# Performance work log

Hardware: AMD Instinct MI355X
Metric: run time of the kernel (lower is better)

The kernel has to match this reference:

```python
import jax, jax.numpy as jnp
import numpy as np

B, S, IN, E, H, NL = 64, 512, 1024, 128, 8, 4
D = E // H  # head dim = 16


def setup_inputs() -> dict:
    key = jax.random.key(0)
    ks = jax.random.split(key, 12)
    rn = lambda k, shape: jax.random.normal(k, shape, jnp.float32) * 0.02
    x = jax.random.normal(ks[0], (B, S, IN), jnp.float32)
    # per-recording valid lengths; recording 0 full-length so no attention key row is all-masked
    lengths = jax.random.randint(ks[1], (B,), 1, S + 1).at[0].set(S)
    key_padding_mask = jnp.arange(S)[None, :] >= lengths[:, None]  # (B,S) True = pad
    return {
        'x': x,
        'key_padding_mask': key_padding_mask,
        'embed_w': rn(ks[2], (IN, E)), 'embed_b': jnp.zeros((E,), jnp.float32),
        'qkv_w': rn(ks[3], (NL, 3, E, E)), 'qkv_b': jnp.zeros((NL, 3, E), jnp.float32),
        'out_w': rn(ks[4], (NL, E, E)), 'out_b': jnp.zeros((NL, E), jnp.float32),
        'ln_g': jnp.ones((NL, E), jnp.float32), 'ln_b': jnp.zeros((NL, E), jnp.float32),
        'ff1_w': rn(ks[5], (NL, E, 4 * E)), 'ff1_b': jnp.zeros((NL, 4 * E), jnp.float32),
        'ff2_w': rn(ks[6], (NL, 4 * E, E)), 'ff2_b': jnp.zeros((NL, E), jnp.float32),
        'fc1_w': rn(ks[7], (E, 32)), 'fc1_b': jnp.zeros((32,), jnp.float32),
        'fc2_w': rn(ks[8], (32, 1)), 'fc2_b': jnp.zeros((1,), jnp.float32),
    }


def _ln(x, g, b):
    m = x.mean(-1, keepdims=True)
    v = x.var(-1, keepdims=True)
    return (x - m) / jnp.sqrt(v + 1e-5) * g + b


def _pos_enc(s, e):
    pos = jnp.arange(s, dtype=jnp.float32)[:, None]
    i = jnp.arange(e)[None, :]
    angle = pos / jnp.power(jnp.float32(10000.0), (2 * (i // 2)).astype(jnp.float32) / e)
    return jnp.where(i % 2 == 0, jnp.sin(angle), jnp.cos(angle))  # (S,E)


def reference(x, key_padding_mask, embed_w, embed_b, qkv_w, qkv_b, out_w, out_b,
              ln_g, ln_b, ff1_w, ff1_b, ff2_w, ff2_b, fc1_w, fc1_b, fc2_w, fc2_b):
    h = x @ embed_w + embed_b  # (B,S,E)
    pe = _pos_enc(S, E)
    scale = 1.0 / jnp.sqrt(jnp.float32(D))
    # module uses batch_first=False MHA on (B,S,E): attention runs across recordings.
    # key_padding_mask.T -> (S,B): masked keys are recordings, per epoch position.
    keymask = key_padding_mask.T[:, None, None, :]  # (S,1,1,B)
    for l in range(NL):
        h = h + pe[None]  # pos enc re-added every block (as in source)
        res = h
        q = (h @ qkv_w[l, 0] + qkv_b[l, 0]).reshape(B, S, H, D)
        k = (h @ qkv_w[l, 1] + qkv_b[l, 1]).reshape(B, S, H, D)
        v = (h @ qkv_w[l, 2] + qkv_b[l, 2]).reshape(B, S, H, D)
        scores = jnp.einsum('ishd,jshd->shij', q, k) * scale  # (S,H,B,B)
        scores = jnp.where(keymask, -jnp.inf, scores)
        attn = jax.nn.softmax(scores, axis=-1)
        o = jnp.einsum('shij,jshd->ishd', attn, v).reshape(B, S, E)
        o = o @ out_w[l] + out_b[l]
        h = _ln(o + res, ln_g[l], ln_b[l])
        res = h
        ffo = jax.nn.relu(h @ ff1_w[l] + ff1_b[l]) @ ff2_w[l] + ff2_b[l]
        h = _ln(ffo + res, ln_g[l], ln_b[l])  # same LN params reused, as in source
    # masked mean pool over epochs (vectorized replacement of the python loop)
    valid = (~key_padding_mask).astype(h.dtype)  # (B,S)
    mean = jnp.einsum('bse,bs->be', h, valid) / valid.sum(axis=1)[:, None]
    out = jax.nn.relu(mean @ fc1_w + fc1_b) @ fc2_w + fc2_b  # (B,1)
    return jax.nn.sigmoid(out)
```

## Files before the change

### kernel.cpp

```cpp
#include <hip/hip_runtime.h>

#define Bb 64
#define Ss 512
#define INn 1024
#define Ee 128
#define Hh 8
#define Dd 16
#define NLl 4

typedef unsigned short u16;
typedef __attribute__((ext_vector_type(8))) short short8;
typedef __attribute__((ext_vector_type(4))) float f32x4;

__device__ __forceinline__ float b2f(unsigned u) { return __uint_as_float(u << 16); }
__device__ __forceinline__ u16 f2b(float f) {
    unsigned u = __float_as_uint(f);
    unsigned r = u + 0x7FFFu + ((u >> 16) & 1u);
    return (u16)(r >> 16);
}
__device__ __forceinline__ uint2 pk4(float4 f) {
    uint2 r;
    r.x = (unsigned)f2b(f.x) | ((unsigned)f2b(f.y) << 16);
    r.y = (unsigned)f2b(f.z) | ((unsigned)f2b(f.w) << 16);
    return r;
}

#define GLOAD_LDS16(g, l) __builtin_amdgcn_global_load_lds( \
    (const __attribute__((address_space(1))) void*)(g),     \
    (__attribute__((address_space(3))) void*)(l), 16, 0, 0)

#define MFMA16(a, b, c) __builtin_amdgcn_mfma_f32_16x16x32_bf16((a), (b), (c), 0, 0, 0)

__global__ __launch_bounds__(256) void prep_kernel(const unsigned char* __restrict__ m,
                                                   int* __restrict__ lengths,
                                                   float* __restrict__ pe,
                                                   const float* __restrict__ ew,
                                                   const float* __restrict__ qw,
                                                   const float* __restrict__ ow,
                                                   const float* __restrict__ f1w,
                                                   const float* __restrict__ f2w,
                                                   u16* __restrict__ we, u16* __restrict__ wq,
                                                   u16* __restrict__ wo, u16* __restrict__ wf1,
                                                   u16* __restrict__ wf2) {
    const int bid = blockIdx.x, tid = threadIdx.x;
    if (bid == 0) {
        __shared__ int lf[3];
        __shared__ int part[256];
        if (tid < 3) lf[tid] = 0;
        __syncthreads();
        int l0 = 0, l1 = 0, l23 = 0;
        for (int i = tid * 128; i < tid * 128 + 128; ++i) {
            if (m[i]) { int md = i & 3; if (md == 0) l0 = 1; else if (md == 1) l1 = 1; else l23 = 1; }
        }
        if (l0) atomicOr(&lf[0], 1);
        if (l1) atomicOr(&lf[1], 1);
        if (l23) atomicOr(&lf[2], 1);
        __syncthreads();
        int enc = lf[1] ? 1 : (lf[2] ? 2 : 0);
        int b = tid >> 2, q = tid & 3, cnt = 0;
        for (int s = q * 128; s < q * 128 + 128; ++s) {
            int idx = b * Ss + s;
            int mm;
            if (enc == 1)      mm = (m[idx] != 0);
            else if (enc == 2) mm = (((const float*)(const void*)m)[idx] != 0.0f);
            else               mm = (((const int*)(const void*)m)[idx] != 0);
            cnt += (mm == 0);
        }
        part[tid] = cnt;
        __syncthreads();
        if (tid < 64)
            lengths[tid] = part[tid * 4] + part[tid * 4 + 1] + part[tid * 4 + 2] + part[tid * 4 + 3];
        return;
    }
    if (bid <= 32) {
        for (int i = tid; i < 2048; i += 256) {
            int idx = (bid - 1) * 2048 + i;
            int s = idx >> 7, e = idx & 127;
            float expo = (float)(2 * (e >> 1)) * (1.0f / 128.0f);
            float freq = powf(10000.0f, -expo);
            float angle = (float)s * freq;
            pe[idx] = (e & 1) ? cosf(angle) : sinf(angle);
        }
        return;
    }
    int tb = bid - 33;
    const float* src; u16* dst; int K, N, tile;
    if (tb < 32)       { src = ew;  dst = we;  K = 1024; N = 128; tile = tb; }
    else if (tb < 80)  { int b = tb - 32;  int mat = b >> 2; src = qw  + (size_t)mat * 16384; dst = wq  + (size_t)mat * 16384; K = 128; N = 128; tile = b & 3; }
    else if (tb < 96)  { int b = tb - 80;  int mat = b >> 2; src = ow  + (size_t)mat * 16384; dst = wo  + (size_t)mat * 16384; K = 128; N = 128; tile = b & 3; }
    else if (tb < 160) { int b = tb - 96;  int mat = b >> 4; src = f1w + (size_t)mat * 65536; dst = wf1 + (size_t)mat * 65536; K = 128; N = 512; tile = b & 15; }
    else               { int b = tb - 160; int mat = b >> 4; src = f2w + (size_t)mat * 65536; dst = wf2 + (size_t)mat * 65536; K = 512; N = 128; tile = b & 15; }
    int ktiles = K >> 6;
    int k0 = (tile % ktiles) * 64, n0 = (tile / ktiles) * 64;
    __shared__ __align__(16) u16 t_s[64 * 68];
    int r = tid >> 2, cq = (tid & 3) * 16;
    const float* sp = src + (size_t)(k0 + r) * N + n0 + cq;
#pragma unroll
    for (int i = 0; i < 4; ++i) {
        float4 f = *(const float4*)(sp + 4 * i);
        *(uint2*)&t_s[r * 68 + cq + 4 * i] = pk4(f);
    }
    __syncthreads();
    u16 tmp[16];
#pragma unroll
    for (int kk = 0; kk < 16; ++kk) tmp[kk] = t_s[(cq + kk) * 68 + r];
    int rowg = n0 + r;
    int x = (rowg & 7) << 3;
    u16* base = dst + (size_t)rowg * K;
    *(uint4*)(base + ((k0 + cq) ^ x))     = ((uint4*)tmp)[0];
    *(uint4*)(base + ((k0 + cq + 8) ^ x)) = ((uint4*)tmp)[1];
}

__global__ __launch_bounds__(256) void embed_gemm(const float* __restrict__ X,
                                                  const u16* __restrict__ Wt,
                                                  const float* __restrict__ bias,
                                                  const float* __restrict__ pe,
                                                  u16* __restrict__ C) {
    __shared__ __align__(16) u16 Af[64 * 68];
    __shared__ __align__(16) u16 Bs[2][128 * 64];
    const int tid = threadIdx.x;
    const int w = tid >> 6, lane = tid & 63, l16 = lane & 15, lhi = lane >> 4;
    const int row0 = blockIdx.x * 64;
    const int xr = (l16 & 7) << 3;
    f32x4 acc[8];
#pragma unroll
    for (int ni = 0; ni < 8; ++ni) acc[ni] = (f32x4){0.f, 0.f, 0.f, 0.f};

    const int ar = tid >> 2, ak = (tid & 3) * 16;
    const int crow = tid >> 3, cc8 = (tid & 7) * 8;
    const int wave_lds = w * 512;
    const u16* Bbase = Wt + cc8;
    const float* Arow = X + (size_t)(row0 + ar) * 1024 + ak;

#pragma unroll
    for (int i = 0; i < 4; ++i)
        GLOAD_LDS16(Bbase + (size_t)(i * 32 + crow) * 1024, &Bs[0][i * 2048 + wave_lds]);

    for (int it = 0; it < 16; ++it) {
        const int k0 = it * 64;
        __syncthreads();
#pragma unroll
        for (int i = 0; i < 4; ++i) {
            float4 f = *(const float4*)(Arow + k0 + 4 * i);
            *(uint2*)&Af[ar * 68 + ak + 4 * i] = pk4(f);
        }
        __syncthreads();
        if (it < 15) {
#pragma unroll
            for (int i = 0; i < 4; ++i)
                GLOAD_LDS16(Bbase + (size_t)(i * 32 + crow) * 1024 + k0 + 64,
                            &Bs[(it + 1) & 1][i * 2048 + wave_lds]);
        }
#pragma unroll
        for (int ks = 0; ks < 2; ++ks) {
            short8 af;
            ((uint2*)&af)[0] = *(const uint2*)&Af[(w * 16 + l16) * 68 + ks * 32 + lhi * 8];
            ((uint2*)&af)[1] = *(const uint2*)&Af[(w * 16 + l16) * 68 + ks * 32 + lhi * 8 + 4];
#pragma unroll
            for (int ni = 0; ni < 8; ++ni) {
                short8 bfr = *(const short8*)&Bs[it & 1][(ni * 16 + l16) * 64 + ((ks * 32 + lhi * 8) ^ xr)];
                acc[ni] = MFMA16(af, bfr, acc[ni]);
            }
        }
    }
    float biasr[8];
#pragma unroll
    for (int ni = 0; ni < 8; ++ni) biasr[ni] = bias[ni * 16 + l16];
#pragma unroll
    for (int reg = 0; reg < 4; ++reg) {
        int r = row0 + w * 16 + lhi * 4 + reg;
        int s = r & 511;
        int bidx = r >> 9;
        int orow = s * 64 + bidx;
        int xo = (bidx & 7) << 3;
        const float* per = pe + (size_t)s * 128;
        u16* crw = C + (size_t)orow * 128;
#pragma unroll
        for (int ni = 0; ni < 8; ++ni) {
            int c = ni * 16 + l16;
            crw[c ^ xo] = f2b(acc[ni][reg] + biasr[ni] + per[c]);
        }
    }
}

__global__ __launch_bounds__(256) void qkv_gemm(const u16* __restrict__ A,
                                                const u16* __restrict__ Wt,
                                                const float* __restrict__ bias,
                                                u16* __restrict__ Cq,
                                                u16* __restrict__ Ckv) {
    __shared__ __align__(16) u16 As[128 * 128];
    __shared__ __align__(16) u16 Bs[128 * 128];
    const int tid = threadIdx.x, w = tid >> 6, lane = tid & 63;
    const int l16 = lane & 15, lhi = lane >> 4;
    const int row0 = blockIdx.x * 128, col0 = blockIdx.y * 128;
    const int so = w * 512 + lane * 8;
    const int xr = (l16 & 7) << 3;
#pragma unroll
    for (int i = 0; i < 8; ++i) {
        GLOAD_LDS16(A + (size_t)row0 * 128 + i * 2048 + so, &As[i * 2048 + w * 512]);
        GLOAD_LDS16(Wt + (size_t)col0 * 128 + i * 2048 + so, &Bs[i * 2048 + w * 512]);
    }
    __syncthreads();
    f32x4 acc[2][8];
#pragma unroll
    for (int mi = 0; mi < 2; ++mi)
#pragma unroll
        for (int ni = 0; ni < 8; ++ni) acc[mi][ni] = (f32x4){0.f, 0.f, 0.f, 0.f};
#pragma unroll
    for (int ks = 0; ks < 4; ++ks) {
        const int ko = (ks * 32 + lhi * 8) ^ xr;
        short8 af[2], bfr[8];
#pragma unroll
        for (int mi = 0; mi < 2; ++mi)
            af[mi] = *(const short8*)&As[(w * 32 + mi * 16 + l16) * 128 + ko];
#pragma unroll
        for (int ni = 0; ni < 8; ++ni)
            bfr[ni] = *(const short8*)&Bs[(ni * 16 + l16) * 128 + ko];
#pragma unroll
        for (int mi = 0; mi < 2; ++mi)
#pragma unroll
            for (int ni = 0; ni < 8; ++ni)
                acc[mi][ni] = MFMA16(af[mi], bfr[ni], acc[mi][ni]);
    }
    float biasr[8];
#pragma unroll
    for (int ni = 0; ni < 8; ++ni) biasr[ni] = bias[col0 + ni * 16 + l16];
#pragma unroll
    for (int mi = 0; mi < 2; ++mi)
#pragma unroll
        for (int reg = 0; reg < 4; ++reg) {
            int r = row0 + w * 32 + mi * 16 + lhi * 4 + reg;
            u16* crw; int cbase;
            if (col0 == 0) { crw = Cq + (size_t)r * 128; cbase = 0; }
            else           { crw = Ckv + (size_t)r * 256; cbase = col0 - 128; }
#pragma unroll
            for (int ni = 0; ni < 8; ++ni)
                crw[cbase + ni * 16 + l16] = f2b(acc[mi][ni][reg] + biasr[ni]);
        }
}

__global__ __launch_bounds__(256) void attnout_kernel(const u16* __restrict__ qb,
                                                      const u16* __restrict__ kvb,
                                                      const u16* __restrict__ wo,
                                                      const float* __restrict__ outb,
                                                      const int* __restrict__ lengths,
                                                      const float* __restrict__ gamma,
                                                      const float* __restrict__ beta,
                                                      u16* __restrict__ h) {
    const int s = blockIdx.x;
    const int tid = threadIdx.x, w = tid >> 6, lane = tid & 63;
    const int l16 = lane & 15, lhi = lane >> 4;
    __shared__ __align__(16) u16 Ps[4 * 64 * 72];
    __shared__ __align__(16) u16 o_s[64 * 136];
    __shared__ int len_s[64];

    if (tid < 64) len_s[tid] = lengths[tid];
    __syncthreads();

    bool mk[4];
#pragma unroll
    for (int jt = 0; jt < 4; ++jt) mk[jt] = (s >= len_s[jt * 16 + l16]);

    u16* pw = Ps + w * 4608;
#pragma unroll
    for (int hp = 0; hp < 2; ++hp) {
        const int hh = w * 2 + hp;
        short8 af[4];
#pragma unroll
        for (int it = 0; it < 4; ++it) {
            af[it] = (short8){0, 0, 0, 0, 0, 0, 0, 0};
            if (lhi < 2)
                af[it] = *(const short8*)(qb + ((size_t)(s * 64 + it * 16 + l16)) * 128 + hh * 16 + lhi * 8);
        }
        f32x4 sf[4][4];
#pragma unroll
        for (int jt = 0; jt < 4; ++jt) {
            short8 bf = (short8){0, 0, 0, 0, 0, 0, 0, 0};
            if (lhi < 2)
                bf = *(const short8*)(kvb + ((size_t)(s * 64 + jt * 16 + l16)) * 256 + hh * 16 + lhi * 8);
#pragma unroll
            for (int it = 0; it < 4; ++it) {
                f32x4 z = {0.f, 0.f, 0.f, 0.f};
                sf[it][jt] = MFMA16(af[it], bf, z);
            }
        }
        float inv[4][4];
#pragma unroll
        for (int it = 0; it < 4; ++it) {
#pragma unroll
            for (int reg = 0; reg < 4; ++reg) {
                float vv[4], mx = -1e30f;
#pragma unroll
                for (int jt = 0; jt < 4; ++jt) {
                    float xv = mk[jt] ? -1e30f : sf[it][jt][reg] * 0.25f;
                    vv[jt] = xv; mx = fmaxf(mx, xv);
                }
                mx = fmaxf(mx, __shfl_xor(mx, 1)); mx = fmaxf(mx, __shfl_xor(mx, 2));
                mx = fmaxf(mx, __shfl_xor(mx, 4)); mx = fmaxf(mx, __shfl_xor(mx, 8));
                float e4[4], sum = 0.f;
#pragma unroll
                for (int jt = 0; jt < 4; ++jt) {
                    float e = mk[jt] ? 0.f : __expf(vv[jt] - mx);
                    e4[jt] = e; sum += e;
                }
                sum += __shfl_xor(sum, 1); sum += __shfl_xor(sum, 2);
                sum += __shfl_xor(sum, 4); sum += __shfl_xor(sum, 8);
                inv[it][reg] = 1.0f / sum;
                int prow = it * 16 + lhi * 4 + reg;
#pragma unroll
                for (int jt = 0; jt < 4; ++jt)
                    pw[prow * 72 + jt * 16 + l16] = f2b(e4[jt]);
            }
        }
        f32x4 ao[4];
#pragma unroll
        for (int it = 0; it < 4; ++it) ao[it] = (f32x4){0.f, 0.f, 0.f, 0.f};
        short8 vb[2];
#pragma unroll
        for (int ksv = 0; ksv < 2; ++ksv)
#pragma unroll
            for (int e = 0; e < 8; ++e)
                vb[ksv][e] = (short)kvb[((size_t)(s * 64 + ksv * 32 + lhi * 8 + e)) * 256
                                        + 128 + hh * 16 + l16];
#pragma unroll
        for (int it = 0; it < 4; ++it)
#pragma unroll
            for (int ksv = 0; ksv < 2; ++ksv) {
                short8 pa = *(const short8*)&pw[(it * 16 + l16) * 72 + ksv * 32 + lhi * 8];
                ao[it] = MFMA16(pa, vb[ksv], ao[it]);
            }
#pragma unroll
        for (int it = 0; it < 4; ++it)
#pragma unroll
            for (int reg = 0; reg < 4; ++reg)
                o_s[(it * 16 + lhi * 4 + reg) * 136 + hh * 16 + l16] = f2b(ao[it][reg] * inv[it][reg]);
    }
    __syncthreads();

    const int xr = (l16 & 7) << 3;
    f32x4 acc[8];
#pragma unroll
    for (int ni = 0; ni < 8; ++ni) acc[ni] = (f32x4){0.f, 0.f, 0.f, 0.f};
#pragma unroll
    for (int ks = 0; ks < 4; ++ks) {
        short8 af = *(const short8*)&o_s[(w * 16 + l16) * 136 + ks * 32 + lhi * 8];
#pragma unroll
        for (int ni = 0; ni < 8; ++ni) {
            short8 bf = *(const short8*)(wo + (size_t)(ni * 16 + l16) * 128 + ((ks * 32 + lhi * 8) ^ xr));
            acc[ni] = MFMA16(af, bf, acc[ni]);
        }
    }
    float biasr[8], gr[8], br[8];
#pragma unroll
    for (int ni = 0; ni < 8; ++ni) {
        int c = ni * 16 + l16;
        biasr[ni] = outb[c]; gr[ni] = gamma[c]; br[ni] = beta[c];
    }
#pragma unroll
    for (int reg = 0; reg < 4; ++reg) {
        int row = w * 16 + lhi * 4 + reg;
        int xo = (row & 7) << 3;
        size_t rbase = ((size_t)(s * 64 + row)) * 128;
        float v[8], sm = 0.f, s2 = 0.f;
#pragma unroll
        for (int ni = 0; ni < 8; ++ni) {
            float x = acc[ni][reg] + biasr[ni] + b2f(h[rbase + ((ni * 16 + l16) ^ xo)]);
            v[ni] = x; sm += x; s2 += x * x;
        }
        sm += __shfl_xor(sm, 1); sm += __shfl_xor(sm, 2);
        sm += __shfl_xor(sm, 4); sm += __shfl_xor(sm, 8);
        s2 += __shfl_xor(s2, 1); s2 += __shfl_xor(s2, 2);
        s2 += __shfl_xor(s2, 4); s2 += __shfl_xor(s2, 8);
        float mean = sm * (1.0f / 128.0f);
        float var = s2 * (1.0f / 128.0f) - mean * mean;
        float rstd = rsqrtf(fmaxf(var, 0.0f) + 1e-5f);
#pragma unroll
        for (int ni = 0; ni < 8; ++ni)
            h[rbase + ((ni * 16 + l16) ^ xo)] = f2b((v[ni] - mean) * rstd * gr[ni] + br[ni]);
    }
}

__global__ __launch_bounds__(256) void ff_fused(const u16* __restrict__ hbuf,
                                                const u16* __restrict__ w1t,
                                                const u16* __restrict__ w2t,
                                                const float* __restrict__ b1,
                                                const float* __restrict__ b2,
                                                const float* __restrict__ gamma,
                                                const float* __restrict__ beta,
                                                const float* __restrict__ pe,
                                                u16* __restrict__ hout) {
    __shared__ __align__(16) u16 A_s[8192];
    __shared__ __align__(16) u16 W1_s[8192];
    __shared__ __align__(16) u16 W2_s[8192];
    __shared__ __align__(16) u16 T_s[4096];
    const int tid = threadIdx.x, w = tid >> 6, lane = tid & 63;
    const int l16 = lane & 15, lhi = lane >> 4;
    const int row0 = blockIdx.x * 64;
    const int so = w * 512 + lane * 8;
    const int xr = (l16 & 7) << 3;

#pragma unroll
    for (int i = 0; i < 4; ++i)
        GLOAD_LDS16(hbuf + (size_t)row0 * 128 + i * 2048 + so, &A_s[i * 2048 + w * 512]);
#pragma unroll
    for (int i = 0; i < 4; ++i) {
        int slot = i * 2048 + so;
        GLOAD_LDS16(w1t + (size_t)(slot >> 7) * 128 + ((slot & 127) ^ (((slot >> 7) & 7) << 3)),
                    &W1_s[slot]);
        GLOAD_LDS16(w2t + (size_t)(slot >> 6) * 512 + ((slot & 63) ^ (((slot >> 6) & 7) << 3)),
                    &W2_s[slot]);
    }
    __syncthreads();

    f32x4 acc2[8];
#pragma unroll
    for (int ni = 0; ni < 8; ++ni) acc2[ni] = (f32x4){0.f, 0.f, 0.f, 0.f};

    for (int nc = 0; nc < 8; ++nc) {
        f32x4 acc1[4];
#pragma unroll
        for (int ni = 0; ni < 4; ++ni) acc1[ni] = (f32x4){0.f, 0.f, 0.f, 0.f};
#pragma unroll
        for (int ks = 0; ks < 4; ++ks) {
            const int ko = (ks * 32 + lhi * 8) ^ xr;
            short8 af = *(const short8*)&A_s[(w * 16 + l16) * 128 + ko];
#pragma unroll
            for (int ni = 0; ni < 4; ++ni) {
                short8 bf = *(const short8*)&W1_s[(ni * 16 + l16) * 128 + ko];
                acc1[ni] = MFMA16(af, bf, acc1[ni]);
            }
        }
        float bb[4];
#pragma unroll
        for (int ni = 0; ni < 4; ++ni) bb[ni] = b1[nc * 64 + ni * 16 + l16];
#pragma unroll
        for (int reg = 0; reg < 4; ++reg) {
            int xt = ((lhi * 4 + reg) & 7) << 3;
#pragma unroll
            for (int ni = 0; ni < 4; ++ni)
                T_s[(w * 16 + lhi * 4 + reg) * 64 + ((ni * 16 + l16) ^ xt)] =
                    f2b(fmaxf(acc1[ni][reg] + bb[ni], 0.0f));
        }
        __syncthreads();
        if (nc < 7) {
#pragma unroll
            for (int i = 0; i < 4; ++i) {
                int slot = i * 2048 + so;
                GLOAD_LDS16(w1t + (size_t)((nc + 1) * 64 + (slot >> 7)) * 128
                                + ((slot & 127) ^ (((slot >> 7) & 7) << 3)),
                            &W1_s[slot]);
            }
        }
#pragma unroll
        for (int ks = 0; ks < 2; ++ks) {
            const int ko = (ks * 32 + lhi * 8) ^ xr;
            short8 pa = *(const short8*)&T_s[(w * 16 + l16) * 64 + ko];
#pragma unroll
            for (int ni = 0; ni < 8; ++ni) {
                short8 bf = *(const short8*)&W2_s[(ni * 16 + l16) * 64 + ko];
                acc2[ni] = MFMA16(pa, bf, acc2[ni]);
            }
        }
        __syncthreads();
        if (nc < 7) {
#pragma unroll
            for (int i = 0; i < 4; ++i) {
                int slot = i * 2048 + so;
                GLOAD_LDS16(w2t + (size_t)(slot >> 6) * 512 + (nc + 1) * 64
                                + ((slot & 63) ^ (((slot >> 6) & 7) << 3)),
                            &W2_s[slot]);
            }
        }
    }
    float b2r[8], gr[8], br[8];
#pragma unroll
    for (int ni = 0; ni < 8; ++ni) {
        int c = ni * 16 + l16;
        b2r[ni] = b2[c]; gr[ni] = gamma[c]; br[ni] = beta[c];
    }
#pragma unroll
    for (int reg = 0; reg < 4; ++reg) {
        int lrow = w * 16 + lhi * 4 + reg;
        int r = row0 + lrow;
        int xo = (lrow & 7) << 3;
        float v[8], sm = 0.f, s2 = 0.f;
#pragma unroll
        for (int ni = 0; ni < 8; ++ni) {
            float x = acc2[ni][reg] + b2r[ni] + b2f(A_s[lrow * 128 + ((ni * 16 + l16) ^ xo)]);
            v[ni] = x; sm += x; s2 += x * x;
        }
        sm += __shfl_xor(sm, 1); sm += __shfl_xor(sm, 2);
        sm += __shfl_xor(sm, 4); sm += __shfl_xor(sm, 8);
        s2 += __shfl_xor(s2, 1); s2 += __shfl_xor(s2, 2);
        s2 += __shfl_xor(s2, 4); s2 += __shfl_xor(s2, 8);
        float mean = sm * (1.0f / 128.0f);
        float var = s2 * (1.0f / 128.0f) - mean * mean;
        float rstd = rsqrtf(fmaxf(var, 0.0f) + 1e-5f);
        u16* crw = hout + (size_t)r * 128;
#pragma unroll
        for (int ni = 0; ni < 8; ++ni) {
            int c = ni * 16 + l16;
            float val = (v[ni] - mean) * rstd * gr[ni] + br[ni];
            if (pe) val += pe[(size_t)(r >> 6) * 128 + c];
            crw[c ^ xo] = f2b(val);
        }
    }
}

__global__ __launch_bounds__(256) void poolhead_kernel(const u16* __restrict__ h,
                                                       const int* __restrict__ lengths,
                                                       const float* __restrict__ fc1w,
                                                       const float* __restrict__ fc1b,
                                                       const float* __restrict__ fc2w,
                                                       const float* __restrict__ fc2b,
                                                       float* __restrict__ out) {
    int b = blockIdx.x, tid = threadIdx.x;
    int e = tid & 127, half = tid >> 7;
    int len = lengths[b];
    int ep = e ^ ((b & 7) << 3);
    float s = 0.0f;
    for (int t = half; t < len; t += 2) s += b2f(h[((size_t)(t * 64 + b)) * 128 + ep]);
    __shared__ float red[256];
    __shared__ float mp[128];
    __shared__ float z[32];
    red[tid] = s;
    __syncthreads();
    if (tid < 128) mp[tid] = (red[tid] + red[tid + 128]) / (float)len;
    __syncthreads();
    if (tid < 32) {
        float a = fc1b[tid];
        for (int k = 0; k < 128; ++k) a = fmaf(mp[k], fc1w[k * 32 + tid], a);
        z[tid] = fmaxf(a, 0.0f);
    }
    __syncthreads();
    if (tid == 0) {
        float a = fc2b[0];
#pragma unroll
        for (int t = 0; t < 32; ++t) a = fmaf(z[t], fc2w[t], a);
        out[b] = 1.0f / (1.0f + expf(-a));
    }
}

extern "C" void kernel_launch(void* const* d_in, const int* in_sizes, int n_in,
                              void* d_out, int out_size, void* d_ws, size_t ws_size,
                              hipStream_t stream) {
    (void)in_sizes; (void)n_in; (void)out_size; (void)ws_size;
    const float* x        = (const float*)d_in[0];
    const unsigned char* mask = (const unsigned char*)d_in[1];
    const float* embed_w  = (const float*)d_in[2];
    const float* embed_b  = (const float*)d_in[3];
    const float* qkv_w    = (const float*)d_in[4];
    const float* qkv_b    = (const float*)d_in[5];
    const float* out_w    = (const float*)d_in[6];
    const float* out_b    = (const float*)d_in[7];
    const float* ln_g     = (const float*)d_in[8];
    const float* ln_b     = (const float*)d_in[9];
    const float* ff1_w    = (const float*)d_in[10];
    const float* ff1_b    = (const float*)d_in[11];
    const float* ff2_w    = (const float*)d_in[12];
    const float* ff2_b    = (const float*)d_in[13];
    const float* fc1_w    = (const float*)d_in[14];
    const float* fc1_b    = (const float*)d_in[15];
    const float* fc2_w    = (const float*)d_in[16];
    const float* fc2_b    = (const float*)d_in[17];

    char* wsb = (char*)d_ws;
    int*   lengths = (int*)wsb;
    float* pe      = (float*)(wsb + 512);
    u16* wt_embed  = (u16*)(wsb + 262656);
    u16* wt_qkv    = (u16*)(wsb + 524800);
    u16* wt_out    = (u16*)(wsb + 918016);
    u16* wt_ff1    = (u16*)(wsb + 1049088);
    u16* wt_ff2    = (u16*)(wsb + 1573376);
    u16* hbuf      = (u16*)(wsb + 2097664);
    u16* qb        = (u16*)(wsb + 10486272);
    u16* kvb       = (u16*)(wsb + 18874880);

    prep_kernel<<<257, 256, 0, stream>>>(mask, lengths, pe,
                                         embed_w, qkv_w, out_w, ff1_w, ff2_w,
                                         wt_embed, wt_qkv, wt_out, wt_ff1, wt_ff2);

    embed_gemm<<<512, 256, 0, stream>>>(x, wt_embed, embed_b, pe, hbuf);

    for (int l = 0; l < NLl; ++l) {
        qkv_gemm<<<dim3(256, 3), 256, 0, stream>>>(
            hbuf, wt_qkv + (size_t)l * 49152, qkv_b + l * 384, qb, kvb);
        attnout_kernel<<<512, 256, 0, stream>>>(
            qb, kvb, wt_out + (size_t)l * 16384, out_b + l * 128,
            lengths, ln_g + l * 128, ln_b + l * 128, hbuf);
        ff_fused<<<512, 256, 0, stream>>>(
            hbuf, wt_ff1 + (size_t)l * 65536, wt_ff2 + (size_t)l * 65536,
            ff1_b + l * 512, ff2_b + l * 128,
            ln_g + l * 128, ln_b + l * 128, (l < 3) ? pe : nullptr, hbuf);
    }

    poolhead_kernel<<<64, 256, 0, stream>>>(hbuf, lengths, fc1_w, fc1_b, fc2_w, fc2_b,
                                            (float*)d_out);
}
```

Measured before the change: 388.5 us.

## Fuse attention/out-proj/LN kernel with feed-forward block into one kernel

Merges the attention+output-projection+LayerNorm kernel with the fused FFN kernel, so the post-attention hidden tile stays in LDS (A_s) rather than being written to and re-read from global memory. Shared memory is overlaid in one arena, and the FFN weight prefetch is issued before the output projection. Block index is remapped to a permuted epoch order, likely for cache or XCD locality. This removes one launch per layer and a global round trip of the hidden state, at the cost of larger LDS use per block and possibly lower occupancy.

```diff
diff --git a/kernel.cpp b/kernel.cpp
--- a/kernel.cpp
+++ b/kernel.cpp
@@ -239,20 +239,34 @@
         }
 }
 
-__global__ __launch_bounds__(256) void attnout_kernel(const u16* __restrict__ qb,
+__global__ __launch_bounds__(256) void attn_ff_kernel(const u16* __restrict__ qb,
                                                       const u16* __restrict__ kvb,
                                                       const u16* __restrict__ wo,
                                                       const float* __restrict__ outb,
+                                                      const u16* __restrict__ w1t,
+                                                      const u16* __restrict__ w2t,
+                                                      const float* __restrict__ b1,
+                                                      const float* __restrict__ b2,
                                                       const int* __restrict__ lengths,
                                                       const float* __restrict__ gamma,
                                                       const float* __restrict__ beta,
+                                                      const float* __restrict__ pe,
                                                       u16* __restrict__ h) {
-    const int s = blockIdx.x;
+    const int d = blockIdx.x;
+    const int s = ((d & 7) << 1) + ((d >> 3) & 1) + ((d >> 4) << 4);
     const int tid = threadIdx.x, w = tid >> 6, lane = tid & 63;
     const int l16 = lane & 15, lhi = lane >> 4;
-    __shared__ __align__(16) u16 Ps[4 * 64 * 72];
-    __shared__ __align__(16) u16 o_s[64 * 136];
+    const int xr = (l16 & 7) << 3;
+    const int so = w * 512 + lane * 8;
+
+    __shared__ __align__(16) u16 arena[39424];
     __shared__ int len_s[64];
+    u16* o_s  = arena;
+    u16* A_s  = arena + 8704;
+    u16* T_s  = arena + 16896;
+    u16* Ps   = arena + 20992;
+    u16* W1_s = arena + 20992;
+    u16* W2_s = arena + 29184;
 
     if (tid < 64) len_s[tid] = lengths[tid];
     __syncthreads();
@@ -337,34 +351,133 @@
     }
     __syncthreads();
 
-    const int xr = (l16 & 7) << 3;
-    f32x4 acc[8];
-#pragma unroll
-    for (int ni = 0; ni < 8; ++ni) acc[ni] = (f32x4){0.f, 0.f, 0.f, 0.f};
-#pragma unroll
-    for (int ks = 0; ks < 4; ++ks) {
-        short8 af = *(const short8*)&o_s[(w * 16 + l16) * 136 + ks * 32 + lhi * 8];
+#pragma unroll
+    for (int i = 0; i < 4; ++i) {
+        int slot = i * 2048 + so;
+        GLOAD_LDS16(w1t + (size_t)(slot >> 7) * 128 + ((slot & 127) ^ (((slot >> 7) & 7) << 3)),
+                    &W1_s[slot]);
+        GLOAD_LDS16(w2t + (size_t)(slot >> 6) * 512 + ((slot & 63) ^ (((slot >> 6) & 7) << 3)),
+                    &W2_s[slot]);
+    }
+
+    {
+        f32x4 acc[8];
+#pragma unroll
+        for (int ni = 0; ni < 8; ++ni) acc[ni] = (f32x4){0.f, 0.f, 0.f, 0.f};
+#pragma unroll
+        for (int ks = 0; ks < 4; ++ks) {
+            short8 af = *(const short8*)&o_s[(w * 16 + l16) * 136 + ks * 32 + lhi * 8];
+#pragma unroll
+            for (int ni = 0; ni < 8; ++ni) {
+                short8 bf = *(const short8*)(wo + (size_t)(ni * 16 + l16) * 128 + ((ks * 32 + lhi * 8) ^ xr));
+                acc[ni] = MFMA16(af, bf, acc[ni]);
+            }
+        }
+        float biasr[8], gr[8], br[8];
 #pragma unroll
         for (int ni = 0; ni < 8; ++ni) {
-            short8 bf = *(const short8*)(wo + (size_t)(ni * 16 + l16) * 128 + ((ks * 32 + lhi * 8) ^ xr));
-            acc[ni] = MFMA16(af, bf, acc[ni]);
-        }
-    }
-    float biasr[8], gr[8], br[8];
+            int c = ni * 16 + l16;
+            biasr[ni] = outb[c]; gr[ni] = gamma[c]; br[ni] = beta[c];
+        }
+#pragma unroll
+        for (int reg = 0; reg < 4; ++reg) {
+            int row = w * 16 + lhi * 4 + reg;
+            int xo = (row & 7) << 3;
+            size_t rbase = ((size_t)(s * 64 + row)) * 128;
+            float v[8], sm = 0.f, s2 = 0.f;
+#pragma unroll
+            for (int ni = 0; ni < 8; ++ni) {
+                float x = acc[ni][reg] + biasr[ni] + b2f(h[rbase + ((ni * 16 + l16) ^ xo)]);
+                v[ni] = x; sm += x; s2 += x * x;
+            }
+            sm += __shfl_xor(sm, 1); sm += __shfl_xor(sm, 2);
+            sm += __shfl_xor(sm, 4); sm += __shfl_xor(sm, 8);
+            s2 += __shfl_xor(s2, 1); s2 += __shfl_xor(s2, 2);
+            s2 += __shfl_xor(s2, 4); s2 += __shfl_xor(s2, 8);
+            float mean = sm * (1.0f / 128.0f);
+            float var = s2 * (1.0f / 128.0f) - mean * mean;
+            float rstd = rsqrtf(fmaxf(var, 0.0f) + 1e-5f);
+#pragma unroll
+            for (int ni = 0; ni < 8; ++ni)
+                A_s[row * 128 + ((ni * 16 + l16) ^ xo)] =
+                    f2b((v[ni] - mean) * rstd * gr[ni] + br[ni]);
+        }
+    }
+    __syncthreads();
+
+    f32x4 acc2[8];
+#pragma unroll
+    for (int ni = 0; ni < 8; ++ni) acc2[ni] = (f32x4){0.f, 0.f, 0.f, 0.f};
+    for (int nc = 0; nc < 8; ++nc) {
+        f32x4 acc1[4];
+#pragma unroll
+        for (int ni = 0; ni < 4; ++ni) acc1[ni] = (f32x4){0.f, 0.f, 0.f, 0.f};
+#pragma unroll
+        for (int ks = 0; ks < 4; ++ks) {
+            const int ko = (ks * 32 + lhi * 8) ^ xr;
+            short8 af = *(const short8*)&A_s[(w * 16 + l16) * 128 + ko];
+#pragma unroll
+            for (int ni = 0; ni < 4; ++ni) {
+                short8 bf = *(const short8*)&W1_s[(ni * 16 + l16) * 128 + ko];
+                acc1[ni] = MFMA16(af, bf, acc1[ni]);
+            }
+        }
+        float bb[4];
+#pragma unroll
+        for (int ni = 0; ni < 4; ++ni) bb[ni] = b1[nc * 64 + ni * 16 + l16];
+#pragma unroll
+        for (int reg = 0; reg < 4; ++reg) {
+            int xt = ((lhi * 4 + reg) & 7) << 3;
+#pragma unroll
+            for (int ni = 0; ni < 4; ++ni)
+                T_s[(w * 16 + lhi * 4 + reg) * 64 + ((ni * 16 + l16) ^ xt)] =
+                    f2b(fmaxf(acc1[ni][reg] + bb[ni], 0.0f));
+        }
+        __syncthreads();
+        if (nc < 7) {
+#pragma unroll
+            for (int i = 0; i < 4; ++i) {
+                int slot = i * 2048 + so;
+                GLOAD_LDS16(w1t + (size_t)((nc + 1) * 64 + (slot >> 7)) * 128
+                                + ((slot & 127) ^ (((slot >> 7) & 7) << 3)),
+                            &W1_s[slot]);
+            }
+        }
+#pragma unroll
+        for (int ks = 0; ks < 2; ++ks) {
+            const int ko = (ks * 32 + lhi * 8) ^ xr;
+            short8 pa = *(const short8*)&T_s[(w * 16 + l16) * 64 + ko];
+#pragma unroll
+            for (int ni = 0; ni < 8; ++ni) {
+                short8 bf = *(const short8*)&W2_s[(ni * 16 + l16) * 64 + ko];
+                acc2[ni] = MFMA16(pa, bf, acc2[ni]);
+            }
+        }
+        __syncthreads();
+        if (nc < 7) {
+#pragma unroll
+            for (int i = 0; i < 4; ++i) {
+                int slot = i * 2048 + so;
+                GLOAD_LDS16(w2t + (size_t)(slot >> 6) * 512 + (nc + 1) * 64
+                                + ((slot & 63) ^ (((slot >> 6) & 7) << 3)),
+                            &W2_s[slot]);
+            }
+        }
+    }
+    float b2r[8], gr[8], br[8];
 #pragma unroll
     for (int ni = 0; ni < 8; ++ni) {
         int c = ni * 16 + l16;
-        biasr[ni] = outb[c]; gr[ni] = gamma[c]; br[ni] = beta[c];
+        b2r[ni] = b2[c]; gr[ni] = gamma[c]; br[ni] = beta[c];
     }
 #pragma unroll
     for (int reg = 0; reg < 4; ++reg) {
-        int row = w * 16 + lhi * 4 + reg;
-        int xo = (row & 7) << 3;
-        size_t rbase = ((size_t)(s * 64 + row)) * 128;
+        int lrow = w * 16 + lhi * 4 + reg;
+        int xo = (lrow & 7) << 3;
         float v[8], sm = 0.f, s2 = 0.f;
 #pragma unroll
         for (int ni = 0; ni < 8; ++ni) {
-            float x = acc[ni][reg] + biasr[ni] + b2f(h[rbase + ((ni * 16 + l16) ^ xo)]);
+            float x = acc2[ni][reg] + b2r[ni] + b2f(A_s[lrow * 128 + ((ni * 16 + l16) ^ xo)]);
             v[ni] = x; sm += x; s2 += x * x;
         }
         sm += __shfl_xor(sm, 1); sm += __shfl_xor(sm, 2);
@@ -374,134 +487,12 @@
         float mean = sm * (1.0f / 128.0f);
         float var = s2 * (1.0f / 128.0f) - mean * mean;
         float rstd = rsqrtf(fmaxf(var, 0.0f) + 1e-5f);
-#pragma unroll
-        for (int ni = 0; ni < 8; ++ni)
-            h[rbase + ((ni * 16 + l16) ^ xo)] = f2b((v[ni] - mean) * rstd * gr[ni] + br[ni]);
-    }
-}
-
-__global__ __launch_bounds__(256) void ff_fused(const u16* __restrict__ hbuf,
-                                                const u16* __restrict__ w1t,
-                                                const u16* __restrict__ w2t,
-                                                const float* __restrict__ b1,
-                                                const float* __restrict__ b2,
-                                                const float* __restrict__ gamma,
-                                                const float* __restrict__ beta,
-                                                const float* __restrict__ pe,
-                                                u16* __restrict__ hout) {
-    __shared__ __align__(16) u16 A_s[8192];
-    __shared__ __align__(16) u16 W1_s[8192];
-    __shared__ __align__(16) u16 W2_s[8192];
-    __shared__ __align__(16) u16 T_s[4096];
-    const int tid = threadIdx.x, w = tid >> 6, lane = tid & 63;
-    const int l16 = lane & 15, lhi = lane >> 4;
-    const int row0 = blockIdx.x * 64;
-    const int so = w * 512 + lane * 8;
-    const int xr = (l16 & 7) << 3;
-
-#pragma unroll
-    for (int i = 0; i < 4; ++i)
-        GLOAD_LDS16(hbuf + (size_t)row0 * 128 + i * 2048 + so, &A_s[i * 2048 + w * 512]);
-#pragma unroll
-    for (int i = 0; i < 4; ++i) {
-        int slot = i * 2048 + so;
-        GLOAD_LDS16(w1t + (size_t)(slot >> 7) * 128 + ((slot & 127) ^ (((slot >> 7) & 7) << 3)),
-                    &W1_s[slot]);
-        GLOAD_LDS16(w2t + (size_t)(slot >> 6) * 512 + ((slot & 63) ^ (((slot >> 6) & 7) << 3)),
-                    &W2_s[slot]);
-    }
-    __syncthreads();
-
-    f32x4 acc2[8];
-#pragma unroll
-    for (int ni = 0; ni < 8; ++ni) acc2[ni] = (f32x4){0.f, 0.f, 0.f, 0.f};
-
-    for (int nc = 0; nc < 8; ++nc) {
-        f32x4 acc1[4];
-#pragma unroll
-        for (int ni = 0; ni < 4; ++ni) acc1[ni] = (f32x4){0.f, 0.f, 0.f, 0.f};
-#pragma unroll
-        for (int ks = 0; ks < 4; ++ks) {
-            const int ko = (ks * 32 + lhi * 8) ^ xr;
-            short8 af = *(const short8*)&A_s[(w * 16 + l16) * 128 + ko];
-#pragma unroll
-            for (int ni = 0; ni < 4; ++ni) {
-                short8 bf = *(const short8*)&W1_s[(ni * 16 + l16) * 128 + ko];
-                acc1[ni] = MFMA16(af, bf, acc1[ni]);
-            }
-        }
-        float bb[4];
-#pragma unroll
-        for (int ni = 0; ni < 4; ++ni) bb[ni] = b1[nc * 64 + ni * 16 + l16];
-#pragma unroll
-        for (int reg = 0; reg < 4; ++reg) {
-            int xt = ((lhi * 4 + reg) & 7) << 3;
-#pragma unroll
-            for (int ni = 0; ni < 4; ++ni)
-                T_s[(w * 16 + lhi * 4 + reg) * 64 + ((ni * 16 + l16) ^ xt)] =
-                    f2b(fmaxf(acc1[ni][reg] + bb[ni], 0.0f));
-        }
-        __syncthreads();
-        if (nc < 7) {
-#pragma unroll
-            for (int i = 0; i < 4; ++i) {
-                int slot = i * 2048 + so;
-                GLOAD_LDS16(w1t + (size_t)((nc + 1) * 64 + (slot >> 7)) * 128
-                                + ((slot & 127) ^ (((slot >> 7) & 7) << 3)),
-                            &W1_s[slot]);
-            }
-        }
-#pragma unroll
-        for (int ks = 0; ks < 2; ++ks) {
-            const int ko = (ks * 32 + lhi * 8) ^ xr;
-            short8 pa = *(const short8*)&T_s[(w * 16 + l16) * 64 + ko];
-#pragma unroll
-            for (int ni = 0; ni < 8; ++ni) {
-                short8 bf = *(const short8*)&W2_s[(ni * 16 + l16) * 64 + ko];
-                acc2[ni] = MFMA16(pa, bf, acc2[ni]);
-            }
-        }
-        __syncthreads();
-        if (nc < 7) {
-#pragma unroll
-            for (int i = 0; i < 4; ++i) {
-                int slot = i * 2048 + so;
-                GLOAD_LDS16(w2t + (size_t)(slot >> 6) * 512 + (nc + 1) * 64
-                                + ((slot & 63) ^ (((slot >> 6) & 7) << 3)),
-                            &W2_s[slot]);
-            }
-        }
-    }
-    float b2r[8], gr[8], br[8];
-#pragma unroll
-    for (int ni = 0; ni < 8; ++ni) {
-        int c = ni * 16 + l16;
-        b2r[ni] = b2[c]; gr[ni] = gamma[c]; br[ni] = beta[c];
-    }
-#pragma unroll
-    for (int reg = 0; reg < 4; ++reg) {
-        int lrow = w * 16 + lhi * 4 + reg;
-        int r = row0 + lrow;
-        int xo = (lrow & 7) << 3;
-        float v[8], sm = 0.f, s2 = 0.f;
-#pragma unroll
-        for (int ni = 0; ni < 8; ++ni) {
-            float x = acc2[ni][reg] + b2r[ni] + b2f(A_s[lrow * 128 + ((ni * 16 + l16) ^ xo)]);
-            v[ni] = x; sm += x; s2 += x * x;
-        }
-        sm += __shfl_xor(sm, 1); sm += __shfl_xor(sm, 2);
-        sm += __shfl_xor(sm, 4); sm += __shfl_xor(sm, 8);
-        s2 += __shfl_xor(s2, 1); s2 += __shfl_xor(s2, 2);
-        s2 += __shfl_xor(s2, 4); s2 += __shfl_xor(s2, 8);
-        float mean = sm * (1.0f / 128.0f);
-        float var = s2 * (1.0f / 128.0f) - mean * mean;
-        float rstd = rsqrtf(fmaxf(var, 0.0f) + 1e-5f);
-        u16* crw = hout + (size_t)r * 128;
+        u16* crw = h + ((size_t)(s * 64 + lrow)) * 128;
 #pragma unroll
         for (int ni = 0; ni < 8; ++ni) {
             int c = ni * 16 + l16;
             float val = (v[ni] - mean) * rstd * gr[ni] + br[ni];
-            if (pe) val += pe[(size_t)(r >> 6) * 128 + c];
+            if (pe) val += pe[(size_t)s * 128 + c];
             crw[c ^ xo] = f2b(val);
         }
     }
@@ -585,13 +576,12 @@
     for (int l = 0; l < NLl; ++l) {
         qkv_gemm<<<dim3(256, 3), 256, 0, stream>>>(
             hbuf, wt_qkv + (size_t)l * 49152, qkv_b + l * 384, qb, kvb);
-        attnout_kernel<<<512, 256, 0, stream>>>(
+        attn_ff_kernel<<<512, 256, 0, stream>>>(
             qb, kvb, wt_out + (size_t)l * 16384, out_b + l * 128,
-            lengths, ln_g + l * 128, ln_b + l * 128, hbuf);
-        ff_fused<<<512, 256, 0, stream>>>(
-            hbuf, wt_ff1 + (size_t)l * 65536, wt_ff2 + (size_t)l * 65536,
+            wt_ff1 + (size_t)l * 65536, wt_ff2 + (size_t)l * 65536,
             ff1_b + l * 512, ff2_b + l * 128,
-            ln_g + l * 128, ln_b + l * 128, (l < 3) ? pe : nullptr, hbuf);
+            lengths, ln_g + l * 128, ln_b + l * 128,
+            (l < 3) ? pe : nullptr, hbuf);
     }
 
     poolhead_kernel<<<64, 256, 0, stream>>>(hbuf, lengths, fc1_w, fc1_b, fc2_w, fc2_b,
```

After: 376.0 us (median of 3 runs). -3.2%, faster.
